# Kernel optimization log

Hardware: AMD Instinct MI355X
Metric: run time of the kernel (lower is better)

## Reference

```python
import jax, jax.numpy as jnp
import numpy as np

NQ = 4          # qubits
NL = 4          # StronglyEntanglingLayers layers (weights.shape[0])
RANGES = [1, 2, 3, 1]  # PennyLane default ranges: (l % (NQ-1)) + 1
B = 1_000_000


def _apply_1q(psi, U, wire):
    # psi: [B,2,2,2,2] complex; U: [2,2] (shared) or [B,2,2] (per-sample)
    psi = jnp.moveaxis(psi, wire + 1, -1)
    if U.ndim == 3:
        psi = jnp.einsum('bji,b...i->b...j', U, psi)
    else:
        psi = jnp.einsum('ji,b...i->b...j', U, psi)
    return jnp.moveaxis(psi, -1, wire + 1)


def _cnot(psi, c, t):
    # flip target axis on the control=1 slice
    psi = jnp.moveaxis(psi, (c + 1, t + 1), (-2, -1))
    psi = jnp.stack([psi[..., 0, :], psi[..., 1, ::-1]], axis=-2)
    return jnp.moveaxis(psi, (-2, -1), (c + 1, t + 1))


def _rot(phi, theta, omega):
    # PennyLane Rot(phi,theta,omega) = RZ(omega) @ RY(theta) @ RZ(phi)
    c = jnp.cos(theta / 2).astype(jnp.complex64)
    s = jnp.sin(theta / 2).astype(jnp.complex64)
    epo = jnp.exp(-0.5j * (phi + omega).astype(jnp.complex64))
    emo = jnp.exp(0.5j * (phi - omega).astype(jnp.complex64))
    a = epo * c
    b = -emo * s
    d = jnp.conj(emo) * s
    e = jnp.conj(epo) * c
    return jnp.stack([jnp.stack([a, b]), jnp.stack([d, e])])  # [2,2]


def _circuit(x, weights):
    # batched 4-qubit state-vector sim; x: [B,4] angles, weights: [4,4,3]
    b = x.shape[0]
    psi = jnp.zeros((b, 2 ** NQ), jnp.complex64).at[:, 0].set(1.0)
    psi = psi.reshape((b,) + (2,) * NQ)
    # RX angle embedding (per-sample gates)
    half = x / 2
    c = jnp.cos(half).astype(jnp.complex64)
    s = (-1j) * jnp.sin(half).astype(jnp.complex64)
    for w in range(NQ):
        U = jnp.stack([jnp.stack([c[:, w], s[:, w]], -1),
                       jnp.stack([s[:, w], c[:, w]], -1)], -2)  # [B,2,2]
        psi = _apply_1q(psi, U, w)
    # StronglyEntanglingLayers: Rot on each wire, then ring of CNOTs
    for l in range(NL):
        for w in range(NQ):
            psi = _apply_1q(psi, _rot(weights[l, w, 0], weights[l, w, 1], weights[l, w, 2]), w)
        r = RANGES[l]
        for w in range(NQ):
            psi = _cnot(psi, w, (w + r) % NQ)
    # PauliZ expvals per wire
    probs = psi.real ** 2 + psi.imag ** 2  # [B,2,2,2,2]
    z = []
    for w in range(NQ):
        axes = tuple(a for a in range(1, NQ + 1) if a != w + 1)
        m = probs.sum(axes)  # [B,2]
        z.append(m[:, 0] - m[:, 1])
    return jnp.stack(z, -1).astype(jnp.float32)  # [B,4]


def setup_inputs() -> dict:
    key = jax.random.key(0)
    k1, k2, k3, k4 = jax.random.split(key, 4)
    x = jax.random.uniform(k1, (B, NQ), jnp.float32)
    weights = jax.random.uniform(k2, (NL, NQ, 3), jnp.float32)  # np.random.rand(4,4,3)
    fc_w = jax.random.normal(k3, (10, NQ), jnp.float32) * 0.5
    fc_b = jax.random.normal(k4, (10,), jnp.float32) * 0.1
    return {"x": x, "weights": weights, "fc_w": fc_w, "fc_b": fc_b}


def reference(x, weights, fc_w, fc_b):
    q = _circuit(x, weights)          # [B,4]
    return q @ fc_w.T + fc_b          # [B,10]
```

## Files before the change

kernel.cpp:

```cpp
#include <hip/hip_runtime.h>

#define NQ 4
#define NL 4

typedef _Float16 f16x8 __attribute__((ext_vector_type(8)));
typedef float f32x16 __attribute__((ext_vector_type(16)));
typedef float f32x4  __attribute__((ext_vector_type(4)));

#define INV2PI 0.15915494309189535f
#define CHUNKS 4
#define CSAMP  256

#define LGKM_BARRIER() do {                                   \
    asm volatile("s_waitcnt lgkmcnt(0)" ::: "memory");        \
    __builtin_amdgcn_sched_barrier(0);                        \
    __builtin_amdgcn_s_barrier();                             \
    __builtin_amdgcn_sched_barrier(0);                        \
  } while (0)

__global__ __launch_bounds__(256) void qnn_fused(
    const float4* __restrict__ x,
    const float*  __restrict__ w,
    const float*  __restrict__ fcw,
    const float*  __restrict__ fcb,
    float*        __restrict__ out,
    int nB)
{
  __shared__ float  sM[512];
  __shared__ float  sG[512];
  __shared__ float4 xbuf[2][CSAMP];
  __shared__ float  obuf[2][CSAMP * 10];

  int t    = threadIdx.x;
  int lane = t & 63;
  int wv   = t >> 6;
  int col  = lane & 31;
  int hi   = lane >> 5;

  {
    int k = t >> 4;
    int j = t & 15;
    int gbase = lane & 48;

    float re = (j == k) ? 1.f : 0.f;
    float im = 0.f;

    const int ranges[4] = {1, 2, 3, 1};
#pragma unroll
    for (int l = 0; l < NL; ++l) {
#pragma unroll
      for (int q = 0; q < NQ; ++q) {
        float phi = w[l*12 + q*3 + 0];
        float th  = w[l*12 + q*3 + 1];
        float om  = w[l*12 + q*3 + 2];
        float st, ct;  __sincosf(0.5f*th, &st, &ct);
        float spo, cpo; __sincosf(0.5f*(phi+om), &spo, &cpo);
        float smo, cmo; __sincosf(0.5f*(phi-om), &smo, &cmo);
        float ar = cpo*ct,  ai = -spo*ct;
        float br = -cmo*st, bi = -smo*st;
        float dr = cmo*st,  di = -smo*st;
        float er = cpo*ct,  ei = spo*ct;

        int m = 8 >> q;
        float pre = __shfl_xor(re, m);
        float pim = __shfl_xor(im, m);
        bool one = (j & m) != 0;
        float scr = one ? er : ar, sci = one ? ei : ai;
        float pcr = one ? dr : br, pci = one ? di : bi;
        float nre = scr*re - sci*im + pcr*pre - pci*pim;
        float nim = scr*im + sci*re + pcr*pim + pci*pre;
        re = nre; im = nim;
      }
      int r = ranges[l];
      int src = j;
#pragma unroll
      for (int q = 3; q >= 0; --q) {
        int mc = 8 >> q;
        int mt = 8 >> ((q + r) & 3);
        src ^= (src & mc) ? mt : 0;
      }
      re = __shfl(re, gbase + src);
      im = __shfl(im, gbase + src);
    }

    int pc = __popc(k) & 3;
    float re2, im2;
    if      (pc == 0) { re2 =  re; im2 =  im; }
    else if (pc == 1) { re2 =  im; im2 = -re; }
    else if (pc == 2) { re2 = -re; im2 = -im; }
    else              { re2 = -im; im2 =  re; }
    sM[j*16 + k]        = re2;
    sM[(16 + j)*16 + k] = im2;

    if (t < 160) {
      int o  = t >> 4;
      int kk = t & 15;
      int jj = (kk & 3) + 8 * ((kk >> 2) & 1) + 4 * (kk >> 3);
      float g = fcw[o*4 + 0] * ((jj & 8) ? -1.f : 1.f)
              + fcw[o*4 + 1] * ((jj & 4) ? -1.f : 1.f)
              + fcw[o*4 + 2] * ((jj & 2) ? -1.f : 1.f)
              + fcw[o*4 + 3] * ((jj & 1) ? -1.f : 1.f);
      sG[t] = g;
    }
    for (int i = t; i < 352; i += 256) sG[160 + i] = 0.f;
  }
  __syncthreads();

  int row = col;
  int k0  = hi * 8;
  f16x8 Ahi, Alo, Ghi;
#pragma unroll
  for (int i = 0; i < 8; ++i) {
    float v = sM[row * 16 + k0 + i];
    _Float16 h = (_Float16)v;
    Ahi[i] = h;
    Alo[i] = (_Float16)(v - (float)h);
    Ghi[i] = (_Float16)sG[row * 16 + k0 + i];
  }

  int o0 = hi * 4;
  float b0 = fcb[o0 + 0], b1 = fcb[o0 + 1], b2 = fcb[o0 + 2], b3 = fcb[o0 + 3];
  float b4 = hi ? 0.f : fcb[8];
  float b5 = hi ? 0.f : fcb[9];

  int base = blockIdx.x * (CHUNKS * CSAMP);
  int lim  = nB * 10;

  {
    int s = base + t;
    float4 pv = x[(s < nB) ? s : (nB - 1)];
    xbuf[0][t] = pv;
  }
  __syncthreads();

#pragma unroll
  for (int c = 0; c < CHUNKS; ++c) {
    float4 nv;
    if (c + 1 < CHUNKS) {
      int s = base + (c + 1) * CSAMP + t;
      nv = x[(s < nB) ? s : (nB - 1)];
    }

    float* ob = obuf[c & 1];

#pragma unroll
    for (int g = 0; g < 2; ++g) {
      int sl = wv * 64 + g * 32 + col;
      float4 xv = xbuf[c & 1][sl];

      float rev0 = xv.x * (0.5f * INV2PI);
      float cs0  = __builtin_amdgcn_sinf(hi ? rev0 : rev0 + 0.25f);
      float rev1 = xv.y * (0.5f * INV2PI);
      float s1 = __builtin_amdgcn_sinf(rev1), c1 = __builtin_amdgcn_cosf(rev1);
      float rev2 = xv.z * (0.5f * INV2PI);
      float s2 = __builtin_amdgcn_sinf(rev2), c2 = __builtin_amdgcn_cosf(rev2);
      float rev3 = xv.w * (0.5f * INV2PI);
      float s3 = __builtin_amdgcn_sinf(rev3), c3 = __builtin_amdgcn_cosf(rev3);

      float a0 = cs0 * c1, a1 = cs0 * s1;
      float w0 = c2 * c3, w1 = c2 * s3, w2 = s2 * c3, w3 = s2 * s3;
      f16x8 Bf;
      Bf[0] = (_Float16)(a0 * w0); Bf[1] = (_Float16)(a0 * w1);
      Bf[2] = (_Float16)(a0 * w2); Bf[3] = (_Float16)(a0 * w3);
      Bf[4] = (_Float16)(a1 * w0); Bf[5] = (_Float16)(a1 * w1);
      Bf[6] = (_Float16)(a1 * w2); Bf[7] = (_Float16)(a1 * w3);

      f32x16 acc = {0.f,0.f,0.f,0.f,0.f,0.f,0.f,0.f,
                    0.f,0.f,0.f,0.f,0.f,0.f,0.f,0.f};
      acc = __builtin_amdgcn_mfma_f32_32x32x16_f16(Ahi, Bf, acc, 0, 0, 0);
      acc = __builtin_amdgcn_mfma_f32_32x32x16_f16(Alo, Bf, acc, 0, 0, 0);

      f16x8 Bp;
      Bp[0] = (_Float16)fmaf(acc[0], acc[0], acc[8]  * acc[8]);
      Bp[1] = (_Float16)fmaf(acc[1], acc[1], acc[9]  * acc[9]);
      Bp[2] = (_Float16)fmaf(acc[2], acc[2], acc[10] * acc[10]);
      Bp[3] = (_Float16)fmaf(acc[3], acc[3], acc[11] * acc[11]);
      Bp[4] = (_Float16)fmaf(acc[4], acc[4], acc[12] * acc[12]);
      Bp[5] = (_Float16)fmaf(acc[5], acc[5], acc[13] * acc[13]);
      Bp[6] = (_Float16)fmaf(acc[6], acc[6], acc[14] * acc[14]);
      Bp[7] = (_Float16)fmaf(acc[7], acc[7], acc[15] * acc[15]);

      f32x16 acc2 = {b0, b1, b2, b3, b4, b5, 0.f, 0.f,
                     0.f, 0.f, 0.f, 0.f, 0.f, 0.f, 0.f, 0.f};
      acc2 = __builtin_amdgcn_mfma_f32_32x32x16_f16(Ghi, Bp, acc2, 0, 0, 0);

      float2 v01; v01.x = acc2[0]; v01.y = acc2[1];
      float2 v23; v23.x = acc2[2]; v23.y = acc2[3];
      *(float2*)&ob[sl * 10 + o0]     = v01;
      *(float2*)&ob[sl * 10 + o0 + 2] = v23;
      if (!hi) {
        float2 v89; v89.x = acc2[4]; v89.y = acc2[5];
        *(float2*)&ob[sl * 10 + 8] = v89;
      }
    }

    if (c + 1 < CHUNKS) {
      xbuf[(c + 1) & 1][t] = nv;
    }
    LGKM_BARRIER();

    int cb = base * 10 + c * (CSAMP * 10);
#pragma unroll
    for (int i = 0; i < 3; ++i) {
      int idx = t + i * 256;
      if (idx < 640) {
        int gidx = cb + idx * 4;
        if (gidx < lim) {
          f32x4 v = *(f32x4*)&ob[idx * 4];
          __builtin_nontemporal_store(v, (f32x4*)&out[gidx]);
        }
      }
    }
  }
}

extern "C" void kernel_launch(void* const* d_in, const int* in_sizes, int n_in,
                              void* d_out, int out_size, void* d_ws, size_t ws_size,
                              hipStream_t stream) {
  const float* x   = (const float*)d_in[0];
  const float* w   = (const float*)d_in[1];
  const float* fcw = (const float*)d_in[2];
  const float* fcb = (const float*)d_in[3];
  float* out = (float*)d_out;
  int nB = in_sizes[0] / 4;

  int nblk = (nB + CHUNKS * CSAMP - 1) / (CHUNKS * CSAMP);
  hipLaunchKernelGGL(qnn_fused, dim3(nblk), dim3(256), 0, stream,
                     (const float4*)x, w, fcw, fcb, out, nB);
}
```

Before: 19.18 us.

## Prefetch all x samples into registers at kernel start, drop LDS staging

```diff
diff --git a/kernel.cpp b/kernel.cpp
--- a/kernel.cpp
+++ b/kernel.cpp
@@ -26,10 +26,9 @@
     float*        __restrict__ out,
     int nB)
 {
-  __shared__ float  sM[512];
-  __shared__ float  sG[512];
-  __shared__ float4 xbuf[2][CSAMP];
-  __shared__ float  obuf[2][CSAMP * 10];
+  __shared__ float sM[512];
+  __shared__ float sG[512];
+  __shared__ float obuf[2][CSAMP * 10];
 
   int t    = threadIdx.x;
   int lane = t & 63;
@@ -37,6 +36,18 @@
   int col  = lane & 31;
   int hi   = lane >> 5;
 
+  int base = blockIdx.x * (CHUNKS * CSAMP);
+
+  float4 xv[CHUNKS][2];
+#pragma unroll
+  for (int c = 0; c < CHUNKS; ++c) {
+#pragma unroll
+    for (int g = 0; g < 2; ++g) {
+      int s = base + c * CSAMP + wv * 64 + g * 32 + col;
+      xv[c][g] = x[(s < nB) ? s : (nB - 1)];
+    }
+  }
+
   {
     int k = t >> 4;
     int j = t & 15;
@@ -53,9 +64,13 @@
         float phi = w[l*12 + q*3 + 0];
         float th  = w[l*12 + q*3 + 1];
         float om  = w[l*12 + q*3 + 2];
-        float st, ct;  __sincosf(0.5f*th, &st, &ct);
-        float spo, cpo; __sincosf(0.5f*(phi+om), &spo, &cpo);
-        float smo, cmo; __sincosf(0.5f*(phi-om), &smo, &cmo);
+        float at = th * (0.5f * INV2PI);
+        float st = __builtin_amdgcn_sinf(at), ct = __builtin_amdgcn_cosf(at);
+        float ap = (phi + om) * (0.5f * INV2PI);
+        float spo = __builtin_amdgcn_sinf(ap), cpo = __builtin_amdgcn_cosf(ap);
+        float am = (phi - om) * (0.5f * INV2PI);
+        float smo = __builtin_amdgcn_sinf(am), cmo = __builtin_amdgcn_cosf(am);
+
         float ar = cpo*ct,  ai = -spo*ct;
         float br = -cmo*st, bi = -smo*st;
         float dr = cmo*st,  di = -smo*st;
@@ -123,38 +138,24 @@
   float b4 = hi ? 0.f : fcb[8];
   float b5 = hi ? 0.f : fcb[9];
 
-  int base = blockIdx.x * (CHUNKS * CSAMP);
-  int lim  = nB * 10;
-
-  {
-    int s = base + t;
-    float4 pv = x[(s < nB) ? s : (nB - 1)];
-    xbuf[0][t] = pv;
-  }
-  __syncthreads();
+  int lim = nB * 10;
 
 #pragma unroll
   for (int c = 0; c < CHUNKS; ++c) {
-    float4 nv;
-    if (c + 1 < CHUNKS) {
-      int s = base + (c + 1) * CSAMP + t;
-      nv = x[(s < nB) ? s : (nB - 1)];
-    }
-
     float* ob = obuf[c & 1];
 
 #pragma unroll
     for (int g = 0; g < 2; ++g) {
       int sl = wv * 64 + g * 32 + col;
-      float4 xv = xbuf[c & 1][sl];
-
-      float rev0 = xv.x * (0.5f * INV2PI);
+      float4 x4 = xv[c][g];
+
+      float rev0 = x4.x * (0.5f * INV2PI);
       float cs0  = __builtin_amdgcn_sinf(hi ? rev0 : rev0 + 0.25f);
-      float rev1 = xv.y * (0.5f * INV2PI);
+      float rev1 = x4.y * (0.5f * INV2PI);
       float s1 = __builtin_amdgcn_sinf(rev1), c1 = __builtin_amdgcn_cosf(rev1);
-      float rev2 = xv.z * (0.5f * INV2PI);
+      float rev2 = x4.z * (0.5f * INV2PI);
       float s2 = __builtin_amdgcn_sinf(rev2), c2 = __builtin_amdgcn_cosf(rev2);
-      float rev3 = xv.w * (0.5f * INV2PI);
+      float rev3 = x4.w * (0.5f * INV2PI);
       float s3 = __builtin_amdgcn_sinf(rev3), c3 = __builtin_amdgcn_cosf(rev3);
 
       float a0 = cs0 * c1, a1 = cs0 * s1;
@@ -194,9 +195,6 @@
       }
     }
 
-    if (c + 1 < CHUNKS) {
-      xbuf[(c + 1) & 1][t] = nv;
-    }
     LGKM_BARRIER();
 
     int cb = base * 10 + c * (CSAMP * 10);
```

After: 18.76 us. 2.2% less time.
